# Kernel optimization log

Measured on AMD Instinct MI355X. Metric: run time of the kernel, lower is better.

Reference implementation:

```python
import jax, jax.numpy as jnp
import numpy as np

B, L, H, V = 256, 2048, 64, 64


def setup_inputs() -> dict:
    key = jax.random.key(0)
    ks = jax.random.split(key, 16)
    s = 0.05
    return {
        "seq": jax.random.randint(ks[0], (B, L), 0, V),
        "embed": jax.random.normal(ks[1], (V, H), jnp.float32) * s,
        "W1": jax.random.normal(ks[2], (2 * H, H), jnp.float32) * s,
        "b1": jnp.zeros((2 * H,), jnp.float32),
        "W2": jax.random.normal(ks[3], (H, 2 * H), jnp.float32) * s,
        "b2": jnp.zeros((H,), jnp.float32),
        "gamma": jnp.ones((H,), jnp.float32),
        "beta": jnp.zeros((H,), jnp.float32),
        "Wk": jax.random.normal(ks[4], (H, H), jnp.float32) * s,
        "Wv": jax.random.normal(ks[5], (H, H), jnp.float32) * s,
        "Wq": jax.random.normal(ks[6], (H, H), jnp.float32) * s,
        "Wrp": jax.random.normal(ks[7], (H, H), jnp.float32) * s,
        "brp": jnp.zeros((H,), jnp.float32),
        "Wout": jax.random.normal(ks[8], (V, H), jnp.float32) * s,
        "bout": jnp.zeros((V,), jnp.float32),
    }


def reference(seq, embed, W1, b1, W2, b2, gamma, beta, Wk, Wv, Wq, Wrp, brp, Wout, bout):
    # encode: LayerNorm(e + FF(e))
    e = embed[seq]                                   # [B, L, H]
    ff = jnp.maximum(e @ W1.T + b1, 0.0) @ W2.T + b2  # [B, L, H]
    h = e + ff
    mu = h.mean(-1, keepdims=True)
    var = ((h - mu) ** 2).mean(-1, keepdims=True)    # torch LN: biased var, eps=1e-5
    hs = (h - mu) / jnp.sqrt(var + 1e-5) * gamma + beta

    # precompute k/v for the first L-1 steps (batched GEMM)
    k_all = hs[:, :-1] @ Wk.T                         # [B, L-1, H]
    v_all = hs[:, :-1] @ Wv.T                         # [B, L-1, H]
    # F.normalize(k, dim=-1): k / max(||k||, 1e-12)
    k_n = k_all / jnp.maximum(jnp.linalg.norm(k_all, axis=-1, keepdims=True), 1e-12)

    def step(M, kv):
        k, v = kv                                      # each [B, H]
        vp = jnp.einsum('bij,bj->bi', M, k)
        M = M + jnp.einsum('bi,bj->bij', v - vp, k)    # rank-1 delta update
        return M, None

    M0 = jnp.zeros((B, H, H), hs.dtype)
    M, _ = jax.lax.scan(step, M0, (jnp.swapaxes(k_n, 0, 1), jnp.swapaxes(v_all, 0, 1)))

    q = hs[:, -1] @ Wq.T                               # [B, H]
    r = jnp.einsum('bij,bj->bi', M, q) @ Wrp.T + brp
    return r @ Wout.T + bout                           # [B, V]
```

## Files before the change

### kernel.cpp

```cpp
#include <hip/hip_runtime.h>


#define DPP_ADD_F32(x, ctrl, rm, bm, bc)                                      \
  (x) = (x) + __int_as_float(__builtin_amdgcn_update_dpp(                     \
            0, __float_as_int(x), (ctrl), (rm), (bm), (bc)))

__device__ __forceinline__ float wave_sum64(float x) {
  DPP_ADD_F32(x, 0x111, 0xf, 0xf, true);
  DPP_ADD_F32(x, 0x112, 0xf, 0xf, true);
  DPP_ADD_F32(x, 0x114, 0xf, 0xf, true);
  DPP_ADD_F32(x, 0x118, 0xf, 0xf, true);
  DPP_ADD_F32(x, 0x142, 0xa, 0xf, false);
  DPP_ADD_F32(x, 0x143, 0xc, 0xf, false);
  return __int_as_float(__builtin_amdgcn_readlane(__float_as_int(x), 63));
}

__device__ __forceinline__ float readlane_f(float x, int lane) {
  return __int_as_float(__builtin_amdgcn_readlane(__float_as_int(x), lane));
}

__global__ __launch_bounds__(64) void build_tables(
    const float* __restrict__ embed, const float* __restrict__ W1,
    const float* __restrict__ b1, const float* __restrict__ W2,
    const float* __restrict__ b2, const float* __restrict__ gamma,
    const float* __restrict__ beta, const float* __restrict__ Wk,
    const float* __restrict__ Wv, const float* __restrict__ Wq,
    float* __restrict__ k_tab, float* __restrict__ v_tab,
    float* __restrict__ q_tab) {
  __shared__ float Wbuf[8448];
  __shared__ float e_s[64];
  __shared__ float f1_s[128];
  __shared__ float hs_s[64];
  const int tok = blockIdx.x;
  const int l = threadIdx.x;

  const float e = embed[tok * 64 + l];
  e_s[l] = e;
  for (int i = 0; i < 128; ++i) Wbuf[i * 65 + l] = W1[i * 64 + l];
  __syncthreads();

  float a0 = b1[l], a1 = b1[l + 64];
#pragma unroll
  for (int h = 0; h < 64; ++h) {
    a0 = fmaf(e_s[h], Wbuf[l * 65 + h], a0);
    a1 = fmaf(e_s[h], Wbuf[(l + 64) * 65 + h], a1);
  }
  f1_s[l] = fmaxf(a0, 0.f);
  f1_s[l + 64] = fmaxf(a1, 0.f);
  __syncthreads();

  for (int i = 0; i < 128; ++i)
    Wbuf[(i >> 1) * 131 + (i & 1) * 64 + l] = W2[i * 64 + l];
  __syncthreads();

  float acc = b2[l];
#pragma unroll
  for (int j = 0; j < 128; ++j) acc = fmaf(f1_s[j], Wbuf[l * 131 + j], acc);
  const float hval = e + acc;

  const float mu = wave_sum64(hval) * (1.f / 64.f);
  const float d = hval - mu;
  const float var = wave_sum64(d * d) * (1.f / 64.f);
  const float hs = d * (1.f / sqrtf(var + 1e-5f)) * gamma[l] + beta[l];
  hs_s[l] = hs;
  __syncthreads();

  for (int i = 0; i < 64; ++i) {
    Wbuf[i * 65 + l] = Wk[i * 64 + l];
    Wbuf[4224 + i * 65 + l] = Wv[i * 64 + l];
  }
  __syncthreads();
  float kk = 0.f, vv = 0.f;
#pragma unroll
  for (int h = 0; h < 64; ++h) {
    kk = fmaf(hs_s[h], Wbuf[l * 65 + h], kk);
    vv = fmaf(hs_s[h], Wbuf[4224 + l * 65 + h], vv);
  }
  __syncthreads();
  for (int i = 0; i < 64; ++i) Wbuf[i * 65 + l] = Wq[i * 64 + l];
  __syncthreads();
  float qq = 0.f;
#pragma unroll
  for (int h = 0; h < 64; ++h) qq = fmaf(hs_s[h], Wbuf[l * 65 + h], qq);

  float nrm = fmaxf(sqrtf(wave_sum64(kk * kk)), 1e-12f);
  k_tab[tok * 64 + l] = kk / nrm;
  v_tab[tok * 64 + l] = vv;
  q_tab[tok * 64 + l] = qq;
}

__global__ __launch_bounds__(64) void build_gram(
    const float* __restrict__ k_tab, const float* __restrict__ q_tab,
    const float* __restrict__ v_tab, float2* __restrict__ GV,
    float* __restrict__ KQ) {
  __shared__ float k_s[4160];
  __shared__ float q_s[64];
  const int a = blockIdx.x;
  const int l = threadIdx.x;
  for (int i = 0; i < 64; ++i) k_s[i * 65 + l] = k_tab[i * 64 + l];
  q_s[l] = q_tab[a * 64 + l];
  __syncthreads();
  float g = 0.f, kq = 0.f;
#pragma unroll
  for (int h = 0; h < 64; ++h) {
    g = fmaf(k_s[a * 65 + h], k_s[l * 65 + h], g);
    kq = fmaf(q_s[h], k_s[l * 65 + h], kq);
  }
  GV[a * 64 + l] = make_float2(g, v_tab[a * 64 + l]);
  KQ[a * 64 + l] = kq;
}

__global__ __launch_bounds__(64, 1) void scan_head(
    const int* __restrict__ seq, const float2* __restrict__ GVg,
    const float* __restrict__ KQ, const float* __restrict__ Wrp,
    const float* __restrict__ brp, const float* __restrict__ Wout,
    const float* __restrict__ bout, float* __restrict__ out) {
  __shared__ float2 GV_s[4160];
  __shared__ float tmp[64];
  const int b = blockIdx.x;
  const int l = threadIdx.x;

#pragma unroll
  for (int i = 0; i < 32; ++i)
    ((float4*)GV_s)[l + 64 * i] = ((const float4*)GVg)[l + 64 * i];
  GV_s[4096 + l] = make_float2(0.f, 0.f);

  const int* tokp = seq + b * 2048;
  int tok_cur = tokp[2047 - l];
  int tok_nxt = tokp[2047 - 64 - l];
  __syncthreads();

  const int qt = __builtin_amdgcn_readlane(tok_cur, 0);
  float y = KQ[qt * 64 + l];
  float r = 0.f;
  if (l == 0) tok_cur = 64;

  float2 gA[64], gB[64];
#pragma unroll
  for (int j = 0; j < 64; ++j) {
    const int bj = __builtin_amdgcn_readlane(tok_cur, j);
    gA[j] = GV_s[bj * 64 + l];
  }

  for (int n = 0; n < 16; ++n) {
    const int i2 = 2 * n + 2, i3 = 2 * n + 3;
    int tok_f1 = (i2 <= 31) ? tokp[2047 - 64 * i2 - l] : 0;
#pragma unroll
    for (int j = 0; j < 64; ++j) {
      const int bn = __builtin_amdgcn_readlane(tok_nxt, j);
      const float2 gv = GV_s[bn * 64 + l];
      const int bc = __builtin_amdgcn_readlane(tok_cur, j) & 63;
      const float s = readlane_f(y, bc);
      y = fmaf(-s, gA[j].x, y);
      r = fmaf(s, gA[j].y, r);
      gB[j] = gv;
    }
    tok_cur = tok_nxt;
    tok_nxt = tok_f1;
    int tok_f2 = (i3 <= 31) ? tokp[2047 - 64 * i3 - l] : 0;
#pragma unroll
    for (int j = 0; j < 64; ++j) {
      const int bn = __builtin_amdgcn_readlane(tok_nxt, j);
      const float2 gv = GV_s[bn * 64 + l];
      const int bc = __builtin_amdgcn_readlane(tok_cur, j) & 63;
      const float s = readlane_f(y, bc);
      y = fmaf(-s, gB[j].x, y);
      r = fmaf(s, gB[j].y, r);
      gA[j] = gv;
    }
    tok_cur = tok_nxt;
    tok_nxt = tok_f2;
  }

  float* Wb = (float*)GV_s;
  tmp[l] = r;
  for (int i = 0; i < 64; ++i) {
    Wb[i * 65 + l] = Wrp[i * 64 + l];
    Wb[4160 + i * 65 + l] = Wout[i * 64 + l];
  }
  __syncthreads();
  float acc = brp[l];
#pragma unroll
  for (int j = 0; j < 64; ++j) acc = fmaf(tmp[j], Wb[l * 65 + j], acc);
  __syncthreads();
  tmp[l] = acc;
  __syncthreads();
  float o = bout[l];
#pragma unroll
  for (int i = 0; i < 64; ++i) o = fmaf(tmp[i], Wb[4160 + l * 65 + i], o);
  out[b * 64 + l] = o;
}

extern "C" void kernel_launch(void* const* d_in, const int* in_sizes, int n_in,
                              void* d_out, int out_size, void* d_ws,
                              size_t ws_size, hipStream_t stream) {
  const int* seq = (const int*)d_in[0];
  const float* embed = (const float*)d_in[1];
  const float* W1 = (const float*)d_in[2];
  const float* b1 = (const float*)d_in[3];
  const float* W2 = (const float*)d_in[4];
  const float* b2 = (const float*)d_in[5];
  const float* gamma = (const float*)d_in[6];
  const float* beta = (const float*)d_in[7];
  const float* Wk = (const float*)d_in[8];
  const float* Wv = (const float*)d_in[9];
  const float* Wq = (const float*)d_in[10];
  const float* Wrp = (const float*)d_in[11];
  const float* brp = (const float*)d_in[12];
  const float* Wout = (const float*)d_in[13];
  const float* bout = (const float*)d_in[14];

  float* wsf = (float*)d_ws;
  float* k_tab = wsf;
  float* v_tab = wsf + 4096;
  float* q_tab = wsf + 8192;
  float2* GV = (float2*)(wsf + 12288);
  float* KQ = wsf + 20480;

  build_tables<<<64, 64, 0, stream>>>(embed, W1, b1, W2, b2, gamma, beta, Wk,
                                      Wv, Wq, k_tab, v_tab, q_tab);
  build_gram<<<64, 64, 0, stream>>>(k_tab, q_tab, v_tab, GV, KQ);
  scan_head<<<256, 64, 0, stream>>>(seq, GV, KQ, Wrp, brp, Wout, bout,
                                    (float*)d_out);
}
```

Before: 133.4 us.

## Shorten scan dependency chain by precomputing lookahead Gram coefficients per step

```diff
diff --git a/kernel.cpp b/kernel.cpp
--- a/kernel.cpp
+++ b/kernel.cpp
@@ -106,7 +106,7 @@
     g = fmaf(k_s[a * 65 + h], k_s[l * 65 + h], g);
     kq = fmaf(q_s[h], k_s[l * 65 + h], kq);
   }
-  GV[a * 64 + l] = make_float2(g, v_tab[a * 64 + l]);
+  GV[a * 64 + l] = make_float2(-g, v_tab[a * 64 + l]);
   KQ[a * 64 + l] = kq;
 }
 
@@ -116,6 +116,7 @@
     const float* __restrict__ brp, const float* __restrict__ Wout,
     const float* __restrict__ bout, float* __restrict__ out) {
   __shared__ float2 GV_s[4160];
+  __shared__ float4 cpk[2064];
   __shared__ float tmp[64];
   const int b = blockIdx.x;
   const int l = threadIdx.x;
@@ -124,53 +125,73 @@
   for (int i = 0; i < 32; ++i)
     ((float4*)GV_s)[l + 64 * i] = ((const float4*)GVg)[l + 64 * i];
   GV_s[4096 + l] = make_float2(0.f, 0.f);
+  if (l < 16) cpk[2048 + l] = make_float4(0.f, 0.f, 0.f, __int_as_float(4096));
 
   const int* tokp = seq + b * 2048;
-  int tok_cur = tokp[2047 - l];
-  int tok_nxt = tokp[2047 - 64 - l];
-  __syncthreads();
-
-  const int qt = __builtin_amdgcn_readlane(tok_cur, 0);
+
+  for (int blk = 0; blk < 32; ++blk) {
+    const int j = blk * 64 + l;
+    int t0 = 64, t1 = 64, t2 = 64, t3 = 64;
+    if (j >= 1) t0 = tokp[2047 - j];
+    if (j >= 2) t1 = tokp[2048 - j];
+    if (j >= 3) t2 = tokp[2049 - j];
+    if (j >= 4) t3 = tokp[2050 - j];
+    float c1 = 0.f, c2 = 0.f, c3 = 0.f;
+    if (t0 < 64) {
+      c1 = GV_s[t1 * 64 + t0].x;
+      c2 = GV_s[t2 * 64 + t0].x;
+      c3 = GV_s[t3 * 64 + t0].x;
+    }
+    cpk[j] = make_float4(c1, c2, c3, __int_as_float(t0 * 64));
+  }
+
+  const int qt = tokp[2047];
   float y = KQ[qt * 64 + l];
   float r = 0.f;
-  if (l == 0) tok_cur = 64;
-
-  float2 gA[64], gB[64];
-#pragma unroll
-  for (int j = 0; j < 64; ++j) {
-    const int bj = __builtin_amdgcn_readlane(tok_cur, j);
-    gA[j] = GV_s[bj * 64 + l];
-  }
-
-  for (int n = 0; n < 16; ++n) {
-    const int i2 = 2 * n + 2, i3 = 2 * n + 3;
-    int tok_f1 = (i2 <= 31) ? tokp[2047 - 64 * i2 - l] : 0;
-#pragma unroll
-    for (int j = 0; j < 64; ++j) {
-      const int bn = __builtin_amdgcn_readlane(tok_nxt, j);
-      const float2 gv = GV_s[bn * 64 + l];
-      const int bc = __builtin_amdgcn_readlane(tok_cur, j) & 63;
-      const float s = readlane_f(y, bc);
-      y = fmaf(-s, gA[j].x, y);
-      r = fmaf(s, gA[j].y, r);
-      gB[j] = gv;
+
+  float4 K[16];
+  float2 C[16];
+  float S[16];
+  float P[16];
+  int tks[16];
+#pragma unroll
+  for (int i = 0; i < 16; ++i) {
+    S[i] = 0.f;
+    P[i] = 0.f;
+    C[i] = make_float2(0.f, 0.f);
+    tks[i] = 4096;
+  }
+#pragma unroll
+  for (int i = 0; i < 12; ++i) K[i] = cpk[i];
+#pragma unroll
+  for (int i = 0; i < 5; ++i)
+    tks[i] = __builtin_amdgcn_readfirstlane(__float_as_int(K[i].w));
+#pragma unroll
+  for (int i = 0; i < 5; ++i) C[i] = GV_s[tks[i] + l];
+  float pP = readlane_f(y, (tks[0] >> 6) & 63);
+
+  for (int n = 0; n < 2048; n += 16) {
+#pragma unroll
+    for (int u = 0; u < 16; ++u) {
+      const int j = n + u;
+      const int m = j & 15;
+      K[(j + 12) & 15] = cpk[j + 12];
+      tks[(j + 5) & 15] =
+          __builtin_amdgcn_readfirstlane(__float_as_int(K[(j + 5) & 15].w));
+      const float p1 = readlane_f(y, (tks[(j + 1) & 15] >> 6) & 63);
+      C[(j + 5) & 15] = GV_s[tks[(j + 5) & 15] + l];
+      const float sj = fmaf(K[m].x, S[(j - 1) & 15], P[m]) + pP;
+      S[m] = sj;
+      pP = p1;
+      P[(j + 3) & 15] = K[(j + 3) & 15].z * sj;
+      P[(j + 2) & 15] = fmaf(K[(j + 2) & 15].y, sj, P[(j + 2) & 15]);
+      const float s2 = S[(j - 2) & 15];
+      y = fmaf(s2, C[(j - 2) & 15].x, y);
+      r = fmaf(s2, C[(j - 2) & 15].y, r);
     }
-    tok_cur = tok_nxt;
-    tok_nxt = tok_f1;
-    int tok_f2 = (i3 <= 31) ? tokp[2047 - 64 * i3 - l] : 0;
-#pragma unroll
-    for (int j = 0; j < 64; ++j) {
-      const int bn = __builtin_amdgcn_readlane(tok_nxt, j);
-      const float2 gv = GV_s[bn * 64 + l];
-      const int bc = __builtin_amdgcn_readlane(tok_cur, j) & 63;
-      const float s = readlane_f(y, bc);
-      y = fmaf(-s, gB[j].x, y);
-      r = fmaf(s, gB[j].y, r);
-      gA[j] = gv;
-    }
-    tok_cur = tok_nxt;
-    tok_nxt = tok_f2;
-  }
+  }
+  r = fmaf(S[2046 & 15], C[2046 & 15].y, r);
+  r = fmaf(S[2047 & 15], C[2047 & 15].y, r);
 
   float* Wb = (float*)GV_s;
   tmp[l] = r;
```

Result: slower. 176.2 us (+32.1%).

## Block the Gram-recurrence scan into 64-step chunks with a local triangular solve

Applied to the files above, without the earlier changes.

```diff
diff --git a/kernel.cpp b/kernel.cpp
--- a/kernel.cpp
+++ b/kernel.cpp
@@ -106,7 +106,7 @@
     g = fmaf(k_s[a * 65 + h], k_s[l * 65 + h], g);
     kq = fmaf(q_s[h], k_s[l * 65 + h], kq);
   }
-  GV[a * 64 + l] = make_float2(g, v_tab[a * 64 + l]);
+  GV[a * 64 + l] = make_float2(-g, v_tab[a * 64 + l]);
   KQ[a * 64 + l] = kq;
 }
 
@@ -116,6 +116,7 @@
     const float* __restrict__ brp, const float* __restrict__ Wout,
     const float* __restrict__ bout, float* __restrict__ out) {
   __shared__ float2 GV_s[4160];
+  __shared__ float G32_s[4225];
   __shared__ float tmp[64];
   const int b = blockIdx.x;
   const int l = threadIdx.x;
@@ -125,51 +126,63 @@
     ((float4*)GV_s)[l + 64 * i] = ((const float4*)GVg)[l + 64 * i];
   GV_s[4096 + l] = make_float2(0.f, 0.f);
 
+#pragma unroll 8
+  for (int i = 0; i < 64; ++i) G32_s[i * 65 + l] = GV_s[i * 64 + l].x;
+  G32_s[64 * 65 + l] = 0.f;
+  G32_s[l * 65 + 64] = 0.f;
+  if (l == 0) G32_s[64 * 65 + 64] = 0.f;
+  __syncthreads();
+
   const int* tokp = seq + b * 2048;
-  int tok_cur = tokp[2047 - l];
-  int tok_nxt = tokp[2047 - 64 - l];
-  __syncthreads();
-
-  const int qt = __builtin_amdgcn_readlane(tok_cur, 0);
+  const int qt = tokp[2047];
   float y = KQ[qt * 64 + l];
   float r = 0.f;
-  if (l == 0) tok_cur = 64;
-
-  float2 gA[64], gB[64];
-#pragma unroll
-  for (int j = 0; j < 64; ++j) {
-    const int bj = __builtin_amdgcn_readlane(tok_cur, j);
-    gA[j] = GV_s[bj * 64 + l];
-  }
+
+  int tokA = tokp[2047 - l];
+  if (l == 0) tokA = 64;
+  int rowA = tokA * 65;
+  int tokB = tokp[2047 - 64 - l];
+  int rowB = tokB * 65;
+
+  float g_pre[8];
+  float2 gv_pre[8];
+#pragma unroll
+  for (int i = 0; i < 8; ++i) {
+    const int st = __builtin_amdgcn_readlane(tokA, i);
+    g_pre[i] = G32_s[rowA + st];
+    gv_pre[i] = GV_s[st * 64 + l];
+  }
+
+  auto body = [&](int tkC, int rwC, int tkN, int rwN) {
+    float cur = __int_as_float(__builtin_amdgcn_ds_bpermute(
+        (tkC & 63) << 2, __float_as_int(y)));
+#pragma unroll
+    for (int i = 0; i < 64; ++i) {
+      const float gi = g_pre[i & 7];
+      const float2 gvi = gv_pre[i & 7];
+      const int ip = i + 8;
+      const int st = (ip < 64) ? __builtin_amdgcn_readlane(tkC, ip)
+                               : __builtin_amdgcn_readlane(tkN, ip & 63);
+      g_pre[i & 7] = G32_s[(ip < 64 ? rwC : rwN) + st];
+      gv_pre[i & 7] = GV_s[st * 64 + l];
+      const float s = readlane_f(cur, i);
+      cur = fmaf(s, gi, cur);
+      y = fmaf(s, gvi.x, y);
+      r = fmaf(s, gvi.y, r);
+    }
+  };
 
   for (int n = 0; n < 16; ++n) {
-    const int i2 = 2 * n + 2, i3 = 2 * n + 3;
-    int tok_f1 = (i2 <= 31) ? tokp[2047 - 64 * i2 - l] : 0;
-#pragma unroll
-    for (int j = 0; j < 64; ++j) {
-      const int bn = __builtin_amdgcn_readlane(tok_nxt, j);
-      const float2 gv = GV_s[bn * 64 + l];
-      const int bc = __builtin_amdgcn_readlane(tok_cur, j) & 63;
-      const float s = readlane_f(y, bc);
-      y = fmaf(-s, gA[j].x, y);
-      r = fmaf(s, gA[j].y, r);
-      gB[j] = gv;
-    }
-    tok_cur = tok_nxt;
-    tok_nxt = tok_f1;
-    int tok_f2 = (i3 <= 31) ? tokp[2047 - 64 * i3 - l] : 0;
-#pragma unroll
-    for (int j = 0; j < 64; ++j) {
-      const int bn = __builtin_amdgcn_readlane(tok_nxt, j);
-      const float2 gv = GV_s[bn * 64 + l];
-      const int bc = __builtin_amdgcn_readlane(tok_cur, j) & 63;
-      const float s = readlane_f(y, bc);
-      y = fmaf(-s, gB[j].x, y);
-      r = fmaf(s, gB[j].y, r);
-      gA[j] = gv;
-    }
-    tok_cur = tok_nxt;
-    tok_nxt = tok_f2;
+    int tokC = (n < 15) ? tokp[2047 - 64 * (2 * n + 2) - l] : 64;
+    body(tokA, rowA, tokB, rowB);
+    const int rowC = tokC * 65;
+    int tokD = (n < 15) ? tokp[2047 - 64 * (2 * n + 3) - l] : 64;
+    body(tokB, rowB, tokC, rowC);
+    const int rowD = tokD * 65;
+    tokA = tokC;
+    rowA = rowC;
+    tokB = tokD;
+    rowB = rowD;
   }
 
   float* Wb = (float*)GV_s;
```

Measured after the change: 149.1 us. 11.8% more time.

## Break scan dependency chain with one-step lookahead readlane and shallower register prefetch

Applied to the files above, without the earlier changes.

```diff
diff --git a/kernel.cpp b/kernel.cpp
--- a/kernel.cpp
+++ b/kernel.cpp
@@ -106,7 +106,7 @@
     g = fmaf(k_s[a * 65 + h], k_s[l * 65 + h], g);
     kq = fmaf(q_s[h], k_s[l * 65 + h], kq);
   }
-  GV[a * 64 + l] = make_float2(g, v_tab[a * 64 + l]);
+  GV[a * 64 + l] = make_float2(-g, v_tab[a * 64 + l]);
   KQ[a * 64 + l] = kq;
 }
 
@@ -124,56 +124,65 @@
   for (int i = 0; i < 32; ++i)
     ((float4*)GV_s)[l + 64 * i] = ((const float4*)GVg)[l + 64 * i];
   GV_s[4096 + l] = make_float2(0.f, 0.f);
+  __syncthreads();
 
   const int* tokp = seq + b * 2048;
-  int tok_cur = tokp[2047 - l];
-  int tok_nxt = tokp[2047 - 64 - l];
-  __syncthreads();
-
-  const int qt = __builtin_amdgcn_readlane(tok_cur, 0);
+  const int qt = tokp[2047];
   float y = KQ[qt * 64 + l];
   float r = 0.f;
-  if (l == 0) tok_cur = 64;
-
-  float2 gA[64], gB[64];
-#pragma unroll
-  for (int j = 0; j < 64; ++j) {
-    const int bj = __builtin_amdgcn_readlane(tok_cur, j);
-    gA[j] = GV_s[bj * 64 + l];
-  }
-
-  for (int n = 0; n < 16; ++n) {
-    const int i2 = 2 * n + 2, i3 = 2 * n + 3;
-    int tok_f1 = (i2 <= 31) ? tokp[2047 - 64 * i2 - l] : 0;
-#pragma unroll
-    for (int j = 0; j < 64; ++j) {
-      const int bn = __builtin_amdgcn_readlane(tok_nxt, j);
-      const float2 gv = GV_s[bn * 64 + l];
-      const int bc = __builtin_amdgcn_readlane(tok_cur, j) & 63;
-      const float s = readlane_f(y, bc);
-      y = fmaf(-s, gA[j].x, y);
-      r = fmaf(s, gA[j].y, r);
-      gB[j] = gv;
+
+  int tokA = (l == 0) ? 64 : tokp[2047 - l];
+  int tokB = tokp[2047 - 64 - l];
+
+  float2 colX[8], colY[8];
+  int selX[8], selY[8];
+
+#pragma unroll
+  for (int k = 0; k < 8; ++k) {
+    selX[k] = __builtin_amdgcn_readlane(tokA, k);
+    colX[k] = GV_s[selX[k] * 64 + l];
+  }
+  float s_prev = 0.f;
+  float cf_cur = 0.f;
+  float p_cur = readlane_f(y, selX[0] & 63);
+
+  auto BATCH = [&](float2 (&cC)[8], int (&sC)[8], float2 (&cN)[8],
+                   int (&sN)[8], int tokvec, int lane_base) {
+#pragma unroll
+    for (int k = 0; k < 8; ++k) {
+      sN[k] = __builtin_amdgcn_readlane(tokvec, lane_base + k);
+      cN[k] = GV_s[sN[k] * 64 + l];
     }
-    tok_cur = tok_nxt;
-    tok_nxt = tok_f1;
-    int tok_f2 = (i3 <= 31) ? tokp[2047 - 64 * i3 - l] : 0;
-#pragma unroll
-    for (int j = 0; j < 64; ++j) {
-      const int bn = __builtin_amdgcn_readlane(tok_nxt, j);
-      const float2 gv = GV_s[bn * 64 + l];
-      const int bc = __builtin_amdgcn_readlane(tok_cur, j) & 63;
-      const float s = readlane_f(y, bc);
-      y = fmaf(-s, gB[j].x, y);
-      r = fmaf(s, gB[j].y, r);
-      gA[j] = gv;
+#pragma unroll
+    for (int k = 0; k < 8; ++k) {
+      const int nsel = ((k < 7) ? sC[k + 1] : sN[0]) & 63;
+      const float p_next = readlane_f(y, nsel);
+      const float s_i = fmaf(cf_cur, s_prev, p_cur);
+      const float cf_next = readlane_f(cC[k].x, nsel);
+      y = fmaf(s_i, cC[k].x, y);
+      r = fmaf(s_i, cC[k].y, r);
+      p_cur = p_next;
+      cf_cur = cf_next;
+      s_prev = s_i;
     }
-    tok_cur = tok_nxt;
-    tok_nxt = tok_f2;
+  };
+
+  for (int blk = 0; blk < 32; ++blk) {
+    BATCH(colX, selX, colY, selY, tokA, 8);
+    BATCH(colY, selY, colX, selX, tokA, 16);
+    BATCH(colX, selX, colY, selY, tokA, 24);
+    BATCH(colY, selY, colX, selX, tokA, 32);
+    BATCH(colX, selX, colY, selY, tokA, 40);
+    BATCH(colY, selY, colX, selX, tokA, 48);
+    BATCH(colX, selX, colY, selY, tokA, 56);
+    BATCH(colY, selY, colX, selX, tokB, 0);
+    tokA = tokB;
+    tokB = (blk + 2 < 32) ? tokp[2047 - 64 * (blk + 2) - l] : 64;
   }
 
   float* Wb = (float*)GV_s;
   tmp[l] = r;
+  __syncthreads();
   for (int i = 0; i < 64; ++i) {
     Wb[i * 65 + l] = Wrp[i * 64 + l];
     Wb[4160 + i * 65 + l] = Wout[i * 64 + l];
```

Measured after the change: 148.7 us. 11.5% more time.
